# Optimization experiments

Measured on AMD Instinct MI355X. Metric: run time of the kernel, lower is better.

Reference implementation:

```python
import jax, jax.numpy as jnp
import numpy as np

B, L, D_IN, D_OUT, H = 4, 2048, 1024, 1024, 16
DH = D_OUT // H
EPS = 1e-6


def setup_inputs() -> dict:
    key = jax.random.key(0)
    ks = jax.random.split(key, 12)
    s_in = 1.0 / np.sqrt(D_IN)
    s_out = 1.0 / np.sqrt(D_OUT)
    return {
        "x": jax.random.normal(ks[0], (B, L, D_IN), jnp.float32),
        "Wq": jax.random.normal(ks[1], (D_OUT, D_IN), jnp.float32) * s_in,
        "Wk": jax.random.normal(ks[2], (D_OUT, D_IN), jnp.float32) * s_in,
        "Wv": jax.random.normal(ks[3], (D_OUT, D_IN), jnp.float32) * s_in,
        "Wg": jax.random.normal(ks[4], (D_OUT, D_IN), jnp.float32) * s_in,
        "Wb": jax.random.normal(ks[5], (D_OUT, D_IN), jnp.float32) * s_in,
        "Wa": jax.random.normal(ks[6], (H, D_IN), jnp.float32) * s_in,
        "dt_bias": jnp.ones((H,), jnp.float32),
        "A_log": jnp.log(jax.random.uniform(ks[7], (H,), jnp.float32, 1e-3, 16.0)),
        "norm_w": jnp.ones((DH,), jnp.float32),
        "Wo": jax.random.normal(ks[8], (D_OUT, D_OUT), jnp.float32) * s_out,
        "bo": jnp.zeros((D_OUT,), jnp.float32),
    }


def _rmsnorm(x, w):
    var = jnp.mean(jnp.square(x), axis=-1, keepdims=True)
    return x * jax.lax.rsqrt(var + EPS) * w


def reference(x, Wq, Wk, Wv, Wg, Wb, Wa, dt_bias, A_log, norm_w, Wo, bo):
    b, l, _ = x.shape
    q = (x @ Wq.T).reshape(b, l, H, DH)   # [B,L,H,Dh]
    k = (x @ Wk.T).reshape(b, l, H, DH)
    v = (x @ Wv.T).reshape(b, l, H, DH)
    gate = (x @ Wg.T).reshape(b, l, H, DH)
    beta = jax.nn.sigmoid(x @ Wb.T).reshape(b, l, H, DH)
    # alpha: [B,L,H] decay per head
    alpha = jnp.exp(-jnp.exp(A_log)[None, None, :] * jax.nn.softplus(x @ Wa.T + dt_bias))
    # l2-normalize q,k along head_dim; scale q
    q = q / jnp.linalg.norm(q, axis=-1, keepdims=True) / np.sqrt(DH)
    k = k / jnp.linalg.norm(k, axis=-1, keepdims=True)

    # scan over time: state S [B,H,Dh,Dh]
    def step(S, inp):
        k_t, q_t, v_t, beta_t, a_t = inp  # [B,H,Dh],...,[B,H]
        S = S * a_t[..., None, None]
        kv_mem = jnp.einsum('bhd,bhde->bhe', k_t, S)
        delta = (v_t - kv_mem) * beta_t
        S = S + k_t[..., :, None] * delta[..., None, :]
        y_t = jnp.einsum('bhd,bhde->bhe', q_t, S)
        return S, y_t

    tfirst = lambda a: jnp.moveaxis(a, 1, 0)  # [B,L,...] -> [L,B,...]
    S0 = jnp.zeros((b, H, DH, DH), x.dtype)
    _, ys = jax.lax.scan(step, S0, (tfirst(k), tfirst(q), tfirst(v), tfirst(beta), tfirst(alpha)))
    ys = jnp.moveaxis(ys, 0, 1)  # [B,L,H,Dh]

    ctx = _rmsnorm(ys, norm_w) * jax.nn.silu(gate)
    ctx = ctx.reshape(b, l, D_OUT)
    return ctx @ Wo.T + bo
```

## Files before the change

kernel.cpp:

```cpp
#include <hip/hip_runtime.h>

#define B_   4
#define L_   2048
#define DIN  1024
#define DOUT 1024
#define H_   16
#define DH_  64
#define M_   (B_ * L_)

typedef __bf16 bf16x8 __attribute__((ext_vector_type(8)));
typedef float  f32x4  __attribute__((ext_vector_type(4)));

__device__ __forceinline__ float bf2f(unsigned short u) {
  union { unsigned int i; float f; } x; x.i = ((unsigned int)u) << 16; return x.f;
}
__device__ __forceinline__ unsigned short f2bf(float f) {
  union { float f; unsigned int i; } x; x.f = f;
  unsigned int r = x.i + 0x7FFFu + ((x.i >> 16) & 1u);
  return (unsigned short)(r >> 16);
}

template <int CTRL>
__device__ __forceinline__ float dpp_add(float x) {
  int v = __builtin_amdgcn_update_dpp(0, __float_as_int(x), CTRL, 0xF, 0xF, false);
  return x + __int_as_float(v);
}
__device__ __forceinline__ float row16_allreduce(float x) {
  x = dpp_add<0xB1>(x);
  x = dpp_add<0x4E>(x);
  x = dpp_add<0x124>(x);
  x = dpp_add<0x128>(x);
  return x;
}

__global__ __launch_bounds__(256)
void cast_hilo(const float* __restrict__ in,
               unsigned short* __restrict__ hi,
               unsigned short* __restrict__ lo, int n)
{
  int i = (blockIdx.x * 256 + threadIdx.x) * 8;
  int stride = gridDim.x * 256 * 8;
  for (; i < n; i += stride) {
    float4 a = *(const float4*)(in + i);
    float4 b = *(const float4*)(in + i + 4);
    float v[8] = {a.x, a.y, a.z, a.w, b.x, b.y, b.z, b.w};
    ushort4 h0, h1, l0, l1;
    unsigned short hh[8], ll[8];
#pragma unroll
    for (int j = 0; j < 8; j++) {
      hh[j] = f2bf(v[j]);
      ll[j] = f2bf(v[j] - bf2f(hh[j]));
    }
    h0 = {hh[0], hh[1], hh[2], hh[3]}; h1 = {hh[4], hh[5], hh[6], hh[7]};
    l0 = {ll[0], ll[1], ll[2], ll[3]}; l1 = {ll[4], ll[5], ll[6], ll[7]};
    *(ushort4*)(hi + i) = h0; *(ushort4*)(hi + i + 4) = h1;
    *(ushort4*)(lo + i) = l0; *(ushort4*)(lo + i + 4) = l1;
  }
}

#define LPAD 72
template <typename OutT>
__device__ __forceinline__
void gemm_hilo_core(const unsigned short* __restrict__ Ahi,
                    const unsigned short* __restrict__ Alo,
                    const unsigned short* __restrict__ Whi,
                    const unsigned short* __restrict__ Wlo,
                    OutT* __restrict__ C,
                    const float* __restrict__ bias,
                    int K, int N, int m0, int n0)
{
  __shared__ unsigned short AsH[128][LPAD];
  __shared__ unsigned short AsL[128][LPAD];
  __shared__ unsigned short BsH[128][LPAD];
  __shared__ unsigned short BsL[128][LPAD];
  const int t = threadIdx.x;
  const int w = t >> 6;
  const int lane = t & 63;
  const int wm = (w >> 1) * 64, wn = (w & 1) * 64;
  const int l15 = lane & 15, quad = lane >> 4;

  f32x4 acc[4][4] = {};

  for (int k0 = 0; k0 < K; k0 += 64) {
#pragma unroll
    for (int i = 0; i < 4; i++) {
      int c = t + 256 * i;
      int row = c >> 3;
      int col = (c & 7) * 8;
      size_t ga = (size_t)(m0 + row) * K + k0 + col;
      size_t gb = (size_t)(n0 + row) * K + k0 + col;
      *(uint4*)(&AsH[row][col]) = *(const uint4*)(Ahi + ga);
      *(uint4*)(&AsL[row][col]) = *(const uint4*)(Alo + ga);
      *(uint4*)(&BsH[row][col]) = *(const uint4*)(Whi + gb);
      *(uint4*)(&BsL[row][col]) = *(const uint4*)(Wlo + gb);
    }
    __syncthreads();
#pragma unroll
    for (int kh = 0; kh < 2; kh++) {
      bf16x8 ah[4], al[4], bh[4], bl[4];
#pragma unroll
      for (int i = 0; i < 4; i++) {
        union U { uint4 u; bf16x8 v; } u0, u1, u2, u3;
        u0.u = *(const uint4*)(&AsH[wm + i * 16 + l15][kh * 32 + quad * 8]);
        u1.u = *(const uint4*)(&AsL[wm + i * 16 + l15][kh * 32 + quad * 8]);
        u2.u = *(const uint4*)(&BsH[wn + i * 16 + l15][kh * 32 + quad * 8]);
        u3.u = *(const uint4*)(&BsL[wn + i * 16 + l15][kh * 32 + quad * 8]);
        ah[i] = u0.v; al[i] = u1.v; bh[i] = u2.v; bl[i] = u3.v;
      }
#pragma unroll
      for (int mt = 0; mt < 4; mt++)
#pragma unroll
        for (int nt = 0; nt < 4; nt++) {
          acc[mt][nt] = __builtin_amdgcn_mfma_f32_16x16x32_bf16(ah[mt], bh[nt], acc[mt][nt], 0, 0, 0);
          acc[mt][nt] = __builtin_amdgcn_mfma_f32_16x16x32_bf16(al[mt], bh[nt], acc[mt][nt], 0, 0, 0);
          acc[mt][nt] = __builtin_amdgcn_mfma_f32_16x16x32_bf16(ah[mt], bl[nt], acc[mt][nt], 0, 0, 0);
        }
    }
    __syncthreads();
  }

#pragma unroll
  for (int mt = 0; mt < 4; mt++) {
#pragma unroll
    for (int nt = 0; nt < 4; nt++) {
      int n = n0 + wn + nt * 16 + l15;
      float bv = bias ? bias[n] : 0.0f;
#pragma unroll
      for (int r = 0; r < 4; r++) {
        int m = m0 + wm + mt * 16 + quad * 4 + r;
        C[(size_t)m * N + n] = (OutT)(acc[mt][nt][r] + bv);
      }
    }
  }
}

struct WPtrs {
  const unsigned short* hi[5];
  const unsigned short* lo[5];
};

__global__ __launch_bounds__(256, 2)
void proj_gemm(const unsigned short* __restrict__ xhi,
               const unsigned short* __restrict__ xlo,
               WPtrs wp, float* __restrict__ outbase)
{
  int z = blockIdx.z;
  float* C = outbase + (size_t)z * ((size_t)M_ * DOUT);
  gemm_hilo_core<float>(xhi, xlo, wp.hi[z], wp.lo[z], C, nullptr,
                        DIN, DOUT, blockIdx.x * 128, blockIdx.y * 128);
}

__global__ __launch_bounds__(256, 2)
void final_gemm(const unsigned short* __restrict__ chi,
                const unsigned short* __restrict__ clo,
                const unsigned short* __restrict__ whi,
                const unsigned short* __restrict__ wlo,
                float* __restrict__ out, const float* __restrict__ bias)
{
  gemm_hilo_core<float>(chi, clo, whi, wlo, out, bias,
                        DOUT, DOUT, blockIdx.x * 128, blockIdx.y * 128);
}

__global__ __launch_bounds__(256)
void alpha_kernel(const float* __restrict__ x,
                  const float* __restrict__ Wa,
                  const float* __restrict__ dtb,
                  const float* __restrict__ Alg,
                  float* __restrict__ alpha)
{
  __shared__ float WaS[16 * 1024];
  const int t = threadIdx.x;
#pragma unroll
  for (int i = 0; i < 16; i++) {
    int idx = (t + 256 * i) * 4;
    *(float4*)(&WaS[idx]) = *(const float4*)(Wa + idx);
  }
  __syncthreads();
  const int w = t >> 6, lane = t & 63;
  for (int r = blockIdx.x * 4 + w; r < M_; r += gridDim.x * 4) {
    const float* xr = x + (size_t)r * DIN + lane * 16;
    float xv[16];
#pragma unroll
    for (int j = 0; j < 4; j++) {
      float4 a = *(const float4*)(xr + j * 4);
      xv[j * 4 + 0] = a.x; xv[j * 4 + 1] = a.y; xv[j * 4 + 2] = a.z; xv[j * 4 + 3] = a.w;
    }
#pragma unroll 1
    for (int h = 0; h < 16; h++) {
      const float* wr = &WaS[h * 1024 + lane * 16];
      float p = 0.f;
#pragma unroll
      for (int j = 0; j < 4; j++) {
        float4 b = *(const float4*)(wr + j * 4);
        p += xv[j * 4 + 0] * b.x + xv[j * 4 + 1] * b.y +
             xv[j * 4 + 2] * b.z + xv[j * 4 + 3] * b.w;
      }
#pragma unroll
      for (int o = 32; o >= 1; o >>= 1) p += __shfl_xor(p, o, 64);
      if (lane == h) {
        float z = p + dtb[h];
        float sp = (z > 20.f) ? z : log1pf(expf(z));
        alpha[(size_t)r * 16 + h] = expf(-expf(Alg[h]) * sp);
      }
    }
  }
}

__global__ __launch_bounds__(256)
void qkb_kernel(float* __restrict__ q,
                float* __restrict__ k,
                float* __restrict__ bta)
{
  const int t = threadIdx.x, w = t >> 6, lane = t & 63;
  const int NP = M_ * H_;
  for (int p = blockIdx.x * 4 + w; p < NP; p += gridDim.x * 4) {
    size_t off = (size_t)p * 64 + lane;
    float qv = q[off];
    float kv = k[off];
    float bv = bta[off];
    float qs = qv * qv, ks = kv * kv;
#pragma unroll
    for (int o = 32; o >= 1; o >>= 1) {
      qs += __shfl_xor(qs, o, 64);
      ks += __shfl_xor(ks, o, 64);
    }
    q[off] = qv * rsqrtf(qs) * 0.125f;
    k[off] = kv * rsqrtf(ks);
    bta[off] = 1.0f / (1.0f + expf(-bv));
  }
}

#define WIN 8
__global__ __launch_bounds__(256, 1)
void scan_kernel(const float* __restrict__ q,
                 const float* __restrict__ k,
                 const float* __restrict__ v,
                 const float* __restrict__ bta,
                 const float* __restrict__ alpha,
                 float* __restrict__ ys)
{
  const int bl = blockIdx.x;
  const int bh = bl & 63;
  const int part = bl >> 6;
  const int b = bh >> 4, h = bh & 15;
  const int w = threadIdx.x >> 6;
  const int lane = threadIdx.x & 63;
  const int g = part * 4 + w;
  const int sg = lane >> 4;
  const int i = lane & 15;
  const int e = g * 4 + sg;

  const size_t rowstride = 1024;
  const size_t bhbase = (size_t)b * L_ * rowstride + (size_t)h * 64;
  const float* kp = k + bhbase + 4 * i;
  const float* qp = q + bhbase + 4 * i;
  const float* vp = v + bhbase + e;
  const float* bp = bta + bhbase + e;
  const float* ap = alpha + (size_t)b * L_ * 16 + h;

  float4 S = {0.f, 0.f, 0.f, 0.f};
  float Ya = 0.f, Yb = 0.f;

  float4 kA[WIN], qA[WIN]; float vA[WIN], bA[WIN], aA[WIN];
  float4 kB[WIN], qB[WIN]; float vB[WIN], bB[WIN], aB[WIN];

#define LOADW(KX, QX, VX, BX, AX, T0)                                     \
  {                                                                       \
    _Pragma("unroll")                                                     \
    for (int s = 0; s < WIN; s++) {                                       \
      int ts = (T0) + s; if (ts > L_ - 1) ts = L_ - 1;                    \
      size_t o = (size_t)ts * rowstride;                                  \
      KX[s] = *(const float4*)(kp + o);                                   \
      QX[s] = *(const float4*)(qp + o);                                   \
      VX[s] = vp[o]; BX[s] = bp[o]; AX[s] = ap[(size_t)ts * 16];          \
    }                                                                     \
  }

#define COMPW(KX, QX, VX, BX, AX, T0, YACC)                               \
  {                                                                       \
    _Pragma("unroll")                                                     \
    for (int tt = 0; tt < WIN; tt++) {                                    \
      float4 kc = KX[tt], qc = QX[tt];                                    \
      float vc = VX[tt], bc = BX[tt], ac = AX[tt];                        \
      float p = kc.x * S.x + kc.y * S.y + kc.z * S.z + kc.w * S.w;        \
      p = row16_allreduce(p);                                             \
      float delta = (vc - ac * p) * bc;                                   \
      S.x = fmaf(ac, S.x, kc.x * delta);                                  \
      S.y = fmaf(ac, S.y, kc.y * delta);                                  \
      S.z = fmaf(ac, S.z, kc.z * delta);                                  \
      S.w = fmaf(ac, S.w, kc.w * delta);                                  \
      float yp = qc.x * S.x + qc.y * S.y + qc.z * S.z + qc.w * S.w;       \
      yp = row16_allreduce(yp);                                           \
      if (i == tt) YACC = yp;                                             \
    }                                                                     \
    if (i < WIN)                                                          \
      ys[bhbase + (size_t)((T0) + i) * rowstride + e] = YACC;             \
  }

  LOADW(kA, qA, vA, bA, aA, 0);
  for (int w0 = 0; w0 < L_; w0 += 2 * WIN) {
    LOADW(kB, qB, vB, bB, aB, w0 + WIN);
    COMPW(kA, qA, vA, bA, aA, w0, Ya);
    LOADW(kA, qA, vA, bA, aA, w0 + 2 * WIN);
    COMPW(kB, qB, vB, bB, aB, w0 + WIN, Yb);
  }
#undef LOADW
#undef COMPW
}

__global__ __launch_bounds__(256)
void out_gate_kernel(const float* __restrict__ ys,
                     const float* __restrict__ g,
                     const float* __restrict__ norm_w,
                     unsigned short* __restrict__ chi,
                     unsigned short* __restrict__ clo)
{
  const int t = threadIdx.x, w = t >> 6, lane = t & 63;
  const int NP = M_ * H_;
  float nw = norm_w[lane];
  for (int p = blockIdx.x * 4 + w; p < NP; p += gridDim.x * 4) {
    size_t off = (size_t)p * 64 + lane;
    float y = ys[off];
    float gv = g[off];
    float s = y * y;
#pragma unroll
    for (int o = 32; o >= 1; o >>= 1) s += __shfl_xor(s, o, 64);
    float rs = rsqrtf(s * (1.0f / 64.0f) + 1e-6f);
    float silu = gv / (1.0f + expf(-gv));
    float c = y * rs * nw * silu;
    unsigned short hh = f2bf(c);
    chi[off] = hh;
    clo[off] = f2bf(c - bf2f(hh));
  }
}

extern "C" void kernel_launch(void* const* d_in, const int* in_sizes, int n_in,
                              void* d_out, int out_size, void* d_ws, size_t ws_size,
                              hipStream_t stream)
{
  const float* x   = (const float*)d_in[0];
  const float* Wq  = (const float*)d_in[1];
  const float* Wk  = (const float*)d_in[2];
  const float* Wv  = (const float*)d_in[3];
  const float* Wg  = (const float*)d_in[4];
  const float* Wb  = (const float*)d_in[5];
  const float* Wa  = (const float*)d_in[6];
  const float* dtb = (const float*)d_in[7];
  const float* Alg = (const float*)d_in[8];
  const float* nw  = (const float*)d_in[9];
  const float* Wo  = (const float*)d_in[10];
  const float* bo  = (const float*)d_in[11];

  const size_t TSZ = (size_t)M_ * DOUT;
  const size_t WSZ = (size_t)DOUT * DIN;

  float* q    = (float*)d_ws;
  float* k    = q + TSZ;
  float* v    = k + TSZ;
  float* g    = v + TSZ;
  float* bta  = g + TSZ;
  float* ys   = bta + TSZ;
  float* alph = ys + TSZ;
  unsigned short* whl = (unsigned short*)(alph + (size_t)M_ * H_);
  unsigned short* whi[6], *wlo[6];
  for (int j = 0; j < 6; j++) { whi[j] = whl + (size_t)(2 * j) * WSZ; wlo[j] = whl + (size_t)(2 * j + 1) * WSZ; }
  unsigned short* xhi = (unsigned short*)ys;
  unsigned short* xlo = xhi + TSZ;
  unsigned short* chi = (unsigned short*)q;
  unsigned short* clo = chi + TSZ;
  float* outp = (float*)d_out;

  cast_hilo<<<2048, 256, 0, stream>>>(x, xhi, xlo, (int)TSZ);
  cast_hilo<<<512, 256, 0, stream>>>(Wq, whi[0], wlo[0], (int)WSZ);
  cast_hilo<<<512, 256, 0, stream>>>(Wk, whi[1], wlo[1], (int)WSZ);
  cast_hilo<<<512, 256, 0, stream>>>(Wv, whi[2], wlo[2], (int)WSZ);
  cast_hilo<<<512, 256, 0, stream>>>(Wg, whi[3], wlo[3], (int)WSZ);
  cast_hilo<<<512, 256, 0, stream>>>(Wb, whi[4], wlo[4], (int)WSZ);
  cast_hilo<<<512, 256, 0, stream>>>(Wo, whi[5], wlo[5], (int)WSZ);

  WPtrs wp;
  for (int j = 0; j < 5; j++) { wp.hi[j] = whi[j]; wp.lo[j] = wlo[j]; }
  dim3 gp(M_ / 128, DOUT / 128, 5);
  proj_gemm<<<gp, 256, 0, stream>>>(xhi, xlo, wp, q);

  alpha_kernel<<<128, 256, 0, stream>>>(x, Wa, dtb, Alg, alph);
  qkb_kernel<<<1024, 256, 0, stream>>>(q, k, bta);
  scan_kernel<<<256, 256, 0, stream>>>(q, k, v, bta, alph, ys);
  out_gate_kernel<<<1024, 256, 0, stream>>>(ys, g, nw, chi, clo);

  dim3 gf(M_ / 128, DOUT / 128);
  final_gemm<<<gf, 256, 0, stream>>>(chi, clo, whi[5], wlo[5], outp, bo);
}
```

Measured before the change: 918.9 us.

## Defer state update by one step to overlap both scan reductions

Reformulates the delta-rule recurrence so each step reduces k·S and q·S against the state from the previous step. Both row reductions are issued together instead of back to back, which shortens the serial dependency chain per timestep. The correction terms need per-step dot products (k_t·k_{t-1}, q_t·k_{t-1}, q_t·k_t), so a new precompute kernel produces them into the output buffer as scratch. The cost is an extra kernel, extra loads and registers in the scan, and a different floating-point association order.

After: 984.2 us. +7.1%, slower.

```diff
diff --git a/kernel.cpp b/kernel.cpp
--- a/kernel.cpp
+++ b/kernel.cpp
@@ -230,6 +230,32 @@
   }
 }
 
+__global__ __launch_bounds__(256)
+void precomp_kernel(const float* __restrict__ q,
+                    const float* __restrict__ k,
+                    float* __restrict__ pc)
+{
+  const int t = threadIdx.x, w = t >> 6, lane = t & 63;
+  const int NP = M_ * H_;
+  for (int p = blockIdx.x * 4 + w; p < NP; p += gridDim.x * 4) {
+    int r = p >> 4;
+    size_t off = (size_t)p * 64 + lane;
+    size_t offm = (r > 0) ? (off - 1024) : off;
+    float kc = k[off], qc = q[off], km = k[offm];
+    float kk1 = kc * km, qk1 = qc * km, qk0 = qc * kc;
+#pragma unroll
+    for (int o = 32; o >= 1; o >>= 1) {
+      kk1 += __shfl_xor(kk1, o, 64);
+      qk1 += __shfl_xor(qk1, o, 64);
+      qk0 += __shfl_xor(qk0, o, 64);
+    }
+    if (lane == 0) {
+      float4 out = {kk1, qk1, qk0, 0.0f};
+      *(float4*)(pc + (size_t)p * 4) = out;
+    }
+  }
+}
+
 #define WIN 8
 __global__ __launch_bounds__(256, 1)
 void scan_kernel(const float* __restrict__ q,
@@ -237,6 +263,7 @@
                  const float* __restrict__ v,
                  const float* __restrict__ bta,
                  const float* __restrict__ alpha,
+                 const float* __restrict__ pc,
                  float* __restrict__ ys)
 {
   const int bl = blockIdx.x;
@@ -257,14 +284,17 @@
   const float* vp = v + bhbase + e;
   const float* bp = bta + bhbase + e;
   const float* ap = alpha + (size_t)b * L_ * 16 + h;
+  const float* pp = pc + ((size_t)b * L_ * 16 + h) * 4;
 
   float4 S = {0.f, 0.f, 0.f, 0.f};
+  float4 km1 = {0.f, 0.f, 0.f, 0.f};
+  float d1 = 0.f, a1 = 0.f;
   float Ya = 0.f, Yb = 0.f;
 
-  float4 kA[WIN], qA[WIN]; float vA[WIN], bA[WIN], aA[WIN];
-  float4 kB[WIN], qB[WIN]; float vB[WIN], bB[WIN], aB[WIN];
-
-#define LOADW(KX, QX, VX, BX, AX, T0)                                     \
+  float4 kA[WIN], qA[WIN], pA[WIN]; float vA[WIN], bA[WIN], aA[WIN];
+  float4 kB[WIN], qB[WIN], pB[WIN]; float vB[WIN], bB[WIN], aB[WIN];
+
+#define LOADW(KX, QX, VX, BX, AX, PX, T0)                                 \
   {                                                                       \
     _Pragma("unroll")                                                     \
     for (int s = 0; s < WIN; s++) {                                       \
@@ -273,36 +303,44 @@
       KX[s] = *(const float4*)(kp + o);                                   \
       QX[s] = *(const float4*)(qp + o);                                   \
       VX[s] = vp[o]; BX[s] = bp[o]; AX[s] = ap[(size_t)ts * 16];          \
+      PX[s] = *(const float4*)(pp + (size_t)ts * 64);                     \
     }                                                                     \
   }
 
-#define COMPW(KX, QX, VX, BX, AX, T0, YACC)                               \
+#define COMPW(KX, QX, VX, BX, AX, PX, T0, YACC)                           \
   {                                                                       \
     _Pragma("unroll")                                                     \
     for (int tt = 0; tt < WIN; tt++) {                                    \
       float4 kc = KX[tt], qc = QX[tt];                                    \
       float vc = VX[tt], bc = BX[tt], ac = AX[tt];                        \
-      float p = kc.x * S.x + kc.y * S.y + kc.z * S.z + kc.w * S.w;        \
-      p = row16_allreduce(p);                                             \
-      float delta = (vc - ac * p) * bc;                                   \
-      S.x = fmaf(ac, S.x, kc.x * delta);                                  \
-      S.y = fmaf(ac, S.y, kc.y * delta);                                  \
-      S.z = fmaf(ac, S.z, kc.z * delta);                                  \
-      S.w = fmaf(ac, S.w, kc.w * delta);                                  \
-      float yp = qc.x * S.x + qc.y * S.y + qc.z * S.z + qc.w * S.w;       \
-      yp = row16_allreduce(yp);                                           \
-      if (i == tt) YACC = yp;                                             \
+      float4 pv = PX[tt];                                                 \
+                  \
+      float u  = kc.x * S.x + kc.y * S.y + kc.z * S.z + kc.w * S.w;       \
+      float uq = qc.x * S.x + qc.y * S.y + qc.z * S.z + qc.w * S.w;       \
+      u  = row16_allreduce(u);                                            \
+      uq = row16_allreduce(uq);                                           \
+                    \
+      S.x = fmaf(a1, S.x, km1.x * d1);                                    \
+      S.y = fmaf(a1, S.y, km1.y * d1);                                    \
+      S.z = fmaf(a1, S.z, km1.z * d1);                                    \
+      S.w = fmaf(a1, S.w, km1.w * d1);                                    \
+                                    \
+      float p  = fmaf(pv.x, d1, a1 * u);                                  \
+      float dl = fmaf(-(ac * bc), p, vc * bc);                            \
+      float y  = fmaf(pv.z, dl, fmaf(ac * pv.y, d1, (ac * a1) * uq));     \
+      if (i == tt) YACC = y;                                              \
+      d1 = dl; a1 = ac; km1 = kc;                                         \
     }                                                                     \
     if (i < WIN)                                                          \
       ys[bhbase + (size_t)((T0) + i) * rowstride + e] = YACC;             \
   }
 
-  LOADW(kA, qA, vA, bA, aA, 0);
+  LOADW(kA, qA, vA, bA, aA, pA, 0);
   for (int w0 = 0; w0 < L_; w0 += 2 * WIN) {
-    LOADW(kB, qB, vB, bB, aB, w0 + WIN);
-    COMPW(kA, qA, vA, bA, aA, w0, Ya);
-    LOADW(kA, qA, vA, bA, aA, w0 + 2 * WIN);
-    COMPW(kB, qB, vB, bB, aB, w0 + WIN, Yb);
+    LOADW(kB, qB, vB, bB, aB, pB, w0 + WIN);
+    COMPW(kA, qA, vA, bA, aA, pA, w0, Ya);
+    LOADW(kA, qA, vA, bA, aA, pA, w0 + 2 * WIN);
+    COMPW(kB, qB, vB, bB, aB, pB, w0 + WIN, Yb);
   }
 #undef LOADW
 #undef COMPW
@@ -369,6 +407,7 @@
   unsigned short* chi = (unsigned short*)q;
   unsigned short* clo = chi + TSZ;
   float* outp = (float*)d_out;
+  float* pcw  = (float*)d_out;
 
   cast_hilo<<<2048, 256, 0, stream>>>(x, xhi, xlo, (int)TSZ);
   cast_hilo<<<512, 256, 0, stream>>>(Wq, whi[0], wlo[0], (int)WSZ);
@@ -385,7 +424,8 @@
 
   alpha_kernel<<<128, 256, 0, stream>>>(x, Wa, dtb, Alg, alph);
   qkb_kernel<<<1024, 256, 0, stream>>>(q, k, bta);
-  scan_kernel<<<256, 256, 0, stream>>>(q, k, v, bta, alph, ys);
+  precomp_kernel<<<1024, 256, 0, stream>>>(q, k, pcw);
+  scan_kernel<<<256, 256, 0, stream>>>(q, k, v, bta, alph, pcw, ys);
   out_gate_kernel<<<1024, 256, 0, stream>>>(ys, g, nw, chi, clo);
 
   dim3 gf(M_ / 128, DOUT / 128);
```

## Split scan state columns across 32-lane halves and double scan grid

Applied to the files above, without the earlier changes.

The recurrent scan now gives each 32-lane half-wave one state column, with each lane holding two state elements instead of four. The grid doubles to 512 blocks with launch bounds allowing two blocks per CU. The aim is to spread the serial time recurrence over more waves and CUs, shortening each lane's dependent chain. The cost is an extra ds_swizzle step in every cross-lane reduction and twice as many redundant k/q loads.

Measured after the change: 1.026 ms. +11.7%, slower.

```diff
diff --git a/kernel.cpp b/kernel.cpp
--- a/kernel.cpp
+++ b/kernel.cpp
@@ -25,11 +25,12 @@
   int v = __builtin_amdgcn_update_dpp(0, __float_as_int(x), CTRL, 0xF, 0xF, false);
   return x + __int_as_float(v);
 }
-__device__ __forceinline__ float row16_allreduce(float x) {
+__device__ __forceinline__ float row32_allreduce(float x) {
   x = dpp_add<0xB1>(x);
   x = dpp_add<0x4E>(x);
   x = dpp_add<0x124>(x);
   x = dpp_add<0x128>(x);
+  x += __int_as_float(__builtin_amdgcn_ds_swizzle(__float_as_int(x), 0x401F));
   return x;
 }
 
@@ -231,7 +232,7 @@
 }
 
 #define WIN 8
-__global__ __launch_bounds__(256, 1)
+__global__ __launch_bounds__(256, 2)
 void scan_kernel(const float* __restrict__ q,
                  const float* __restrict__ k,
                  const float* __restrict__ v,
@@ -245,24 +246,24 @@
   const int b = bh >> 4, h = bh & 15;
   const int w = threadIdx.x >> 6;
   const int lane = threadIdx.x & 63;
-  const int g = part * 4 + w;
-  const int sg = lane >> 4;
-  const int i = lane & 15;
-  const int e = g * 4 + sg;
+  const int gg = part * 4 + w;
+  const int half = lane >> 5;
+  const int i = lane & 31;
+  const int e = gg * 2 + half;
 
   const size_t rowstride = 1024;
   const size_t bhbase = (size_t)b * L_ * rowstride + (size_t)h * 64;
-  const float* kp = k + bhbase + 4 * i;
-  const float* qp = q + bhbase + 4 * i;
+  const float* kp = k + bhbase + 2 * i;
+  const float* qp = q + bhbase + 2 * i;
   const float* vp = v + bhbase + e;
   const float* bp = bta + bhbase + e;
   const float* ap = alpha + (size_t)b * L_ * 16 + h;
 
-  float4 S = {0.f, 0.f, 0.f, 0.f};
+  float2 S = {0.f, 0.f};
   float Ya = 0.f, Yb = 0.f;
 
-  float4 kA[WIN], qA[WIN]; float vA[WIN], bA[WIN], aA[WIN];
-  float4 kB[WIN], qB[WIN]; float vB[WIN], bB[WIN], aB[WIN];
+  float2 kA[WIN], qA[WIN]; float vA[WIN], bA[WIN], aA[WIN];
+  float2 kB[WIN], qB[WIN]; float vB[WIN], bB[WIN], aB[WIN];
 
 #define LOADW(KX, QX, VX, BX, AX, T0)                                     \
   {                                                                       \
@@ -270,8 +271,8 @@
     for (int s = 0; s < WIN; s++) {                                       \
       int ts = (T0) + s; if (ts > L_ - 1) ts = L_ - 1;                    \
       size_t o = (size_t)ts * rowstride;                                  \
-      KX[s] = *(const float4*)(kp + o);                                   \
-      QX[s] = *(const float4*)(qp + o);                                   \
+      KX[s] = *(const float2*)(kp + o);                                   \
+      QX[s] = *(const float2*)(qp + o);                                   \
       VX[s] = vp[o]; BX[s] = bp[o]; AX[s] = ap[(size_t)ts * 16];          \
     }                                                                     \
   }
@@ -280,17 +281,15 @@
   {                                                                       \
     _Pragma("unroll")                                                     \
     for (int tt = 0; tt < WIN; tt++) {                                    \
-      float4 kc = KX[tt], qc = QX[tt];                                    \
+      float2 kc = KX[tt], qc = QX[tt];                                    \
       float vc = VX[tt], bc = BX[tt], ac = AX[tt];                        \
-      float p = kc.x * S.x + kc.y * S.y + kc.z * S.z + kc.w * S.w;        \
-      p = row16_allreduce(p);                                             \
+      float p = kc.x * S.x + kc.y * S.y;                                  \
+      p = row32_allreduce(p);                                             \
       float delta = (vc - ac * p) * bc;                                   \
       S.x = fmaf(ac, S.x, kc.x * delta);                                  \
       S.y = fmaf(ac, S.y, kc.y * delta);                                  \
-      S.z = fmaf(ac, S.z, kc.z * delta);                                  \
-      S.w = fmaf(ac, S.w, kc.w * delta);                                  \
-      float yp = qc.x * S.x + qc.y * S.y + qc.z * S.z + qc.w * S.w;       \
-      yp = row16_allreduce(yp);                                           \
+      float yp = qc.x * S.x + qc.y * S.y;                                 \
+      yp = row32_allreduce(yp);                                           \
       if (i == tt) YACC = yp;                                             \
     }                                                                     \
     if (i < WIN)                                                          \
@@ -385,7 +384,7 @@
 
   alpha_kernel<<<128, 256, 0, stream>>>(x, Wa, dtb, Alg, alph);
   qkb_kernel<<<1024, 256, 0, stream>>>(q, k, bta);
-  scan_kernel<<<256, 256, 0, stream>>>(q, k, v, bta, alph, ys);
+  scan_kernel<<<512, 256, 0, stream>>>(q, k, v, bta, alph, ys);
   out_gate_kernel<<<1024, 256, 0, stream>>>(ys, g, nw, chi, clo);
 
   dim3 gf(M_ / 128, DOUT / 128);
```

## Replace per-step delta-rule scan with chunked (WY-style) formulation using precomputed tables

Applied to the files above, without the earlier changes.

Adds a chunk_tab_kernel that, for each chunk of 16 timesteps, precomputes the decay-weighted intra-chunk k·k and q·k matrices, the cumulative decay factors and the state-update weights into a table placed in the output buffer. The scan kernel then processes a chunk at a time: it computes the state projections for all 16 steps in parallel, solves the small triangular system for deltas, forms outputs, and applies one rank-16 state update per chunk. This removes most of the serial dependency chain of two cross-lane reductions per timestep. In exchange it adds a kernel, extra table memory traffic and more arithmetic, and reuses d_out as scratch before the final GEMM overwrites it.

Result: slower. 2.775 ms (+202.0%).

```diff
diff --git a/kernel.cpp b/kernel.cpp
--- a/kernel.cpp
+++ b/kernel.cpp
@@ -8,6 +8,10 @@
 #define DH_  64
 #define M_   (B_ * L_)
 
+#define CH_  16
+#define NC_  (L_ / CH_)
+#define TBL  544
+
 typedef __bf16 bf16x8 __attribute__((ext_vector_type(8)));
 typedef float  f32x4  __attribute__((ext_vector_type(4)));
 
@@ -31,6 +35,10 @@
   x = dpp_add<0x124>(x);
   x = dpp_add<0x128>(x);
   return x;
+}
+
+__device__ __forceinline__ float f4c(const float4& v, int j) {
+  return j == 0 ? v.x : j == 1 ? v.y : j == 2 ? v.z : v.w;
 }
 
 __global__ __launch_bounds__(256)
@@ -230,13 +238,68 @@
   }
 }
 
-#define WIN 8
+__global__ __launch_bounds__(256)
+void chunk_tab_kernel(const float* __restrict__ q,
+                      const float* __restrict__ k,
+                      const float* __restrict__ alpha,
+                      float* __restrict__ tab)
+{
+  const int bh = blockIdx.x >> 7;
+  const int c  = blockIdx.x & (NC_ - 1);
+  const int b  = bh >> 4, h = bh & 15;
+  const int tq = threadIdx.x >> 6;
+  const int lane = threadIdx.x & 63;
+  const int sg = lane >> 4;
+  const int i  = lane & 15;
+  const int t  = tq * 4 + sg;
+  const int T0 = c * CH_;
+
+  const size_t rowstride = 1024;
+  const size_t bhbase = (size_t)b * L_ * rowstride + (size_t)h * 64;
+  const float* kp = k + bhbase + 4 * i;
+  const float* qp = q + bhbase + 4 * i;
+  const float* ap = alpha + ((size_t)b * L_ + T0) * 16 + h;
+
+  float a[CH_];
+#pragma unroll
+  for (int j = 0; j < CH_; j++) a[j] = ap[(size_t)j * 16];
+
+  float R[CH_];
+  R[CH_ - 1] = 1.0f;
+#pragma unroll
+  for (int s = CH_ - 2; s >= 0; s--)
+    R[s] = (s >= t) ? 1.0f : a[s + 1] * R[s + 1];
+  float gam = a[0] * R[0];
+
+  float4 kt = *(const float4*)(kp + (size_t)(T0 + t) * rowstride);
+  float4 qt = *(const float4*)(qp + (size_t)(T0 + t) * rowstride);
+
+  float Av = 0.f, Aqv = 0.f, wv = 0.f;
+#pragma unroll
+  for (int s = 0; s < CH_; s++) {
+    float4 ks = *(const float4*)(kp + (size_t)(T0 + s) * rowstride);
+    float pk = kt.x * ks.x + kt.y * ks.y + kt.z * ks.z + kt.w * ks.w;
+    float pq = qt.x * ks.x + qt.y * ks.y + qt.z * ks.z + qt.w * ks.w;
+    pk = row16_allreduce(pk);
+    pq = row16_allreduce(pq);
+    float Ae  = (s < t)  ? R[s] * pk : 0.f;
+    float Aqe = (s <= t) ? R[s] * pq : 0.f;
+    if (i == s) { Av = Ae; Aqv = Aqe; wv = R[s]; }
+  }
+
+  float* tb = tab + ((size_t)bh * NC_ + c) * TBL;
+  tb[t * 16 + i] = Av;
+  tb[256 + t * 16 + i] = Aqv;
+  if (i == 0) tb[512 + t] = gam;
+  if (t == CH_ - 1) tb[528 + i] = wv;
+}
+
 __global__ __launch_bounds__(256, 1)
 void scan_kernel(const float* __restrict__ q,
                  const float* __restrict__ k,
                  const float* __restrict__ v,
                  const float* __restrict__ bta,
-                 const float* __restrict__ alpha,
+                 const float* __restrict__ tab,
                  float* __restrict__ ys)
 {
   const int bl = blockIdx.x;
@@ -256,56 +319,82 @@
   const float* qp = q + bhbase + 4 * i;
   const float* vp = v + bhbase + e;
   const float* bp = bta + bhbase + e;
-  const float* ap = alpha + (size_t)b * L_ * 16 + h;
+  const float* tb = tab + (size_t)bh * NC_ * TBL;
 
   float4 S = {0.f, 0.f, 0.f, 0.f};
-  float Ya = 0.f, Yb = 0.f;
-
-  float4 kA[WIN], qA[WIN]; float vA[WIN], bA[WIN], aA[WIN];
-  float4 kB[WIN], qB[WIN]; float vB[WIN], bB[WIN], aB[WIN];
-
-#define LOADW(KX, QX, VX, BX, AX, T0)                                     \
-  {                                                                       \
-    _Pragma("unroll")                                                     \
-    for (int s = 0; s < WIN; s++) {                                       \
-      int ts = (T0) + s; if (ts > L_ - 1) ts = L_ - 1;                    \
-      size_t o = (size_t)ts * rowstride;                                  \
-      KX[s] = *(const float4*)(kp + o);                                   \
-      QX[s] = *(const float4*)(qp + o);                                   \
-      VX[s] = vp[o]; BX[s] = bp[o]; AX[s] = ap[(size_t)ts * 16];          \
-    }                                                                     \
-  }
-
-#define COMPW(KX, QX, VX, BX, AX, T0, YACC)                               \
-  {                                                                       \
-    _Pragma("unroll")                                                     \
-    for (int tt = 0; tt < WIN; tt++) {                                    \
-      float4 kc = KX[tt], qc = QX[tt];                                    \
-      float vc = VX[tt], bc = BX[tt], ac = AX[tt];                        \
-      float p = kc.x * S.x + kc.y * S.y + kc.z * S.z + kc.w * S.w;        \
-      p = row16_allreduce(p);                                             \
-      float delta = (vc - ac * p) * bc;                                   \
-      S.x = fmaf(ac, S.x, kc.x * delta);                                  \
-      S.y = fmaf(ac, S.y, kc.y * delta);                                  \
-      S.z = fmaf(ac, S.z, kc.z * delta);                                  \
-      S.w = fmaf(ac, S.w, kc.w * delta);                                  \
-      float yp = qc.x * S.x + qc.y * S.y + qc.z * S.z + qc.w * S.w;       \
-      yp = row16_allreduce(yp);                                           \
-      if (i == tt) YACC = yp;                                             \
-    }                                                                     \
-    if (i < WIN)                                                          \
-      ys[bhbase + (size_t)((T0) + i) * rowstride + e] = YACC;             \
-  }
-
-  LOADW(kA, qA, vA, bA, aA, 0);
-  for (int w0 = 0; w0 < L_; w0 += 2 * WIN) {
-    LOADW(kB, qB, vB, bB, aB, w0 + WIN);
-    COMPW(kA, qA, vA, bA, aA, w0, Ya);
-    LOADW(kA, qA, vA, bA, aA, w0 + 2 * WIN);
-    COMPW(kB, qB, vB, bB, aB, w0 + WIN, Yb);
-  }
-#undef LOADW
-#undef COMPW
+
+#pragma unroll 1
+  for (int c = 0; c < NC_; c++, tb += TBL) {
+    const int T0 = c * CH_;
+
+    float4 gm[4], wg[4];
+#pragma unroll
+    for (int j = 0; j < 4; j++) {
+      gm[j] = *(const float4*)(tb + 512 + 4 * j);
+      wg[j] = *(const float4*)(tb + 528 + 4 * j);
+    }
+
+    float4 kc[CH_];
+    float dkg[CH_], dqg[CH_];
+#pragma unroll
+    for (int t = 0; t < CH_; t++) {
+      kc[t] = *(const float4*)(kp + (size_t)(T0 + t) * rowstride);
+      float4 qt = *(const float4*)(qp + (size_t)(T0 + t) * rowstride);
+      float pk = kc[t].x * S.x + kc[t].y * S.y + kc[t].z * S.z + kc[t].w * S.w;
+      float pq = qt.x * S.x + qt.y * S.y + qt.z * S.z + qt.w * S.w;
+      pk = row16_allreduce(pk);
+      pq = row16_allreduce(pq);
+      float gt = f4c(gm[t >> 2], t & 3);
+      dkg[t] = gt * pk;
+      dqg[t] = gt * pq;
+    }
+
+    float dl[CH_];
+#pragma unroll
+    for (int t = 0; t < CH_; t++) {
+      float vc = vp[(size_t)(T0 + t) * rowstride];
+      float bc = bp[(size_t)(T0 + t) * rowstride];
+      float acc = vc - dkg[t];
+#pragma unroll
+      for (int s4 = 0; s4 < (t + 3) / 4; s4++) {
+        float4 Ar = *(const float4*)(tb + t * 16 + 4 * s4);
+#pragma unroll
+        for (int j = 0; j < 4; j++) {
+          int s = 4 * s4 + j;
+          if (s < t) acc -= f4c(Ar, j) * dl[s];
+        }
+      }
+      dl[t] = bc * acc;
+    }
+
+    float Y = 0.f;
+#pragma unroll
+    for (int t = 0; t < CH_; t++) {
+      float yv = dqg[t];
+#pragma unroll
+      for (int s4 = 0; s4 < (t + 4) / 4; s4++) {
+        float4 Ar = *(const float4*)(tb + 256 + t * 16 + 4 * s4);
+#pragma unroll
+        for (int j = 0; j < 4; j++) {
+          int s = 4 * s4 + j;
+          if (s <= t) yv = fmaf(f4c(Ar, j), dl[s], yv);
+        }
+      }
+      if (i == t) Y = yv;
+    }
+    ys[bhbase + (size_t)(T0 + i) * rowstride + e] = Y;
+
+    float g15 = f4c(gm[3], 3);
+    S.x *= g15; S.y *= g15; S.z *= g15; S.w *= g15;
+#pragma unroll
+    for (int s = 0; s < CH_; s++) {
+      float cs = f4c(wg[s >> 2], s & 3) * dl[s];
+      S.x = fmaf(cs, kc[s].x, S.x);
+      S.y = fmaf(cs, kc[s].y, S.y);
+      S.z = fmaf(cs, kc[s].z, S.z);
+      S.w = fmaf(cs, kc[s].w, S.w);
+    }
+  }
 }
 
 __global__ __launch_bounds__(256)
@@ -369,12 +458,13 @@
   unsigned short* chi = (unsigned short*)q;
   unsigned short* clo = chi + TSZ;
   float* outp = (float*)d_out;
+  float* tabw = (float*)d_out;
 
   cast_hilo<<<2048, 256, 0, stream>>>(x, xhi, xlo, (int)TSZ);
   cast_hilo<<<512, 256, 0, stream>>>(Wq, whi[0], wlo[0], (int)WSZ);
   cast_hilo<<<512, 256, 0, stream>>>(Wk, whi[1], wlo[1], (int)WSZ);
+  cast_hilo<<<512, 256, 0, stream>>>(Wg, whi[3], wlo[3], (int)WSZ);
   cast_hilo<<<512, 256, 0, stream>>>(Wv, whi[2], wlo[2], (int)WSZ);
-  cast_hilo<<<512, 256, 0, stream>>>(Wg, whi[3], wlo[3], (int)WSZ);
   cast_hilo<<<512, 256, 0, stream>>>(Wb, whi[4], wlo[4], (int)WSZ);
   cast_hilo<<<512, 256, 0, stream>>>(Wo, whi[5], wlo[5], (int)WSZ);
 
@@ -385,7 +475,8 @@
 
   alpha_kernel<<<128, 256, 0, stream>>>(x, Wa, dtb, Alg, alph);
   qkb_kernel<<<1024, 256, 0, stream>>>(q, k, bta);
-  scan_kernel<<<256, 256, 0, stream>>>(q, k, v, bta, alph, ys);
+  chunk_tab_kernel<<<64 * NC_, 256, 0, stream>>>(q, k, alph, tabw);
+  scan_kernel<<<256, 256, 0, stream>>>(q, k, v, bta, tabw, ys);
   out_gate_kernel<<<1024, 256, 0, stream>>>(ys, g, nw, chi, clo);
 
   dim3 gf(M_ / 128, DOUT / 128);
```
